# Kernel optimization log

Measured on AMD Instinct MI355X. Metric: run time of the kernel, lower is better.

Reference implementation:

```python
import jax, jax.numpy as jnp
import numpy as np

B, L, H, E = 2, 2048, 16, 64
S, D = L, E


def setup_inputs() -> dict:
    key = jax.random.key(0)
    kq, kk, kv = jax.random.split(key, 3)
    queries = jax.random.normal(kq, (B, L, H, E), dtype=jnp.float32)
    keys = jax.random.normal(kk, (B, S, H, E), dtype=jnp.float32)
    values = jax.random.normal(kv, (B, S, H, D), dtype=jnp.float32)
    return {"queries": queries, "keys": keys, "values": values}


def reference(queries, keys, values):
    # FullAttention forward: mask_flag=True, attn_mask=None -> causal mask,
    # scale=None -> 1/sqrt(E), dropout in eval mode (identity).
    Bq, Lq, Hq, Eq = queries.shape
    Sq = values.shape[1]
    scale = 1.0 / jnp.sqrt(jnp.asarray(Eq, dtype=queries.dtype))
    # [B,H,L,S] score matrix, same as torch.einsum('blhe,bshe->bhls', q, k)
    scores = jnp.einsum('blhe,bshe->bhls', queries, keys)
    # TriangularCausalMask: triu(ones, diagonal=1) -> True above diagonal = masked
    causal = jnp.triu(jnp.ones((Lq, Sq), dtype=bool), k=1)
    scores = jnp.where(causal[None, None, :, :], -jnp.inf, scores)
    A = jax.nn.softmax(scale * scores, axis=-1)
    V = jnp.einsum('bhls,bshd->blhd', A, values)
    return V
```

## Files before the change

### kernel.cpp

```cpp
#include <hip/hip_runtime.h>
#include <hip/hip_bf16.h>


#define B_DIM 2
#define L_DIM 2048
#define H_DIM 16
#define E_DIM 64
#define NEG_INF (-1e30f)
#define CAP   16.0f

typedef __attribute__((ext_vector_type(8))) short short8;
typedef __attribute__((ext_vector_type(4))) float ffrag;

static __device__ __forceinline__ short f2bf(float x) {
    __hip_bfloat16 h = __float2bfloat16(x);
    return *reinterpret_cast<short*>(&h);
}
static __device__ __forceinline__ unsigned pk2(float lo, float hi) {
    __hip_bfloat162 h = __float22bfloat162_rn(make_float2(lo, hi));
    return *reinterpret_cast<unsigned*>(&h);
}

__global__ __launch_bounds__(256, 4)
void attn_fused(const float* __restrict__ Q, const float* __restrict__ K,
                const float* __restrict__ V, float* __restrict__ O) {
    const int lid = blockIdx.x;
    const int x   = lid & 7;
    const int c   = (lid >> 3) & 31;
    const int k4  = lid >> 8;
    const int bh  = x * 4 + k4;
    const int b   = bh >> 4;
    const int h   = bh & 15;
    int strip;
    switch (k4) {
        case 0:  strip = c;              break;
        case 1:  strip = 31 - c;         break;
        case 2:  strip = c ^ 16;         break;
        default: strip = 31 - (c ^ 16);  break;
    }
    const int q0 = strip * 64;

    const int tid  = threadIdx.x;
    const int wave = tid >> 6;
    const int lane = tid & 63;
    const int n16  = lane & 15;
    const int quad = lane >> 4;

    __shared__ short Kt[4096];
    __shared__ short Vt[4096];
    __shared__ short Pq[4096];

    const float sc = 0.125f * 1.44269504088896340736f;
    const int gq = q0 + wave * 16 + n16;

    short8 qf[2];
    {
        const float4* pq = (const float4*)(Q + (((size_t)b * L_DIM + gq) * H_DIM + h) * E_DIM);
#pragma unroll
        for (int kt = 0; kt < 2; ++kt) {
            float4 x0 = pq[kt * 8 + quad * 2];
            float4 x1 = pq[kt * 8 + quad * 2 + 1];
            short8 f;
            f[0] = f2bf(x0.x * sc); f[1] = f2bf(x0.y * sc);
            f[2] = f2bf(x0.z * sc); f[3] = f2bf(x0.w * sc);
            f[4] = f2bf(x1.x * sc); f[5] = f2bf(x1.y * sc);
            f[6] = f2bf(x1.z * sc); f[7] = f2bf(x1.w * sc);
            qf[kt] = f;
        }
    }

    const int rr  = tid >> 2;
    const int c2  = tid & 3;
    const int kOff0 = rr * 64 + (((2 * c2)     ^ (rr & 7)) * 8);
    const int kOff1 = rr * 64 + (((2 * c2 + 1) ^ (rr & 7)) * 8);
    const int kp2 = (tid & 31) * 2;
    const int c8  = (tid >> 5) * 8;

    float4 kr[4], va[2], vb2[2];

    auto load_tile = [&](int kt0) {
        const float4* kg = (const float4*)(K + (((size_t)b * L_DIM + kt0 + rr) * H_DIM + h) * E_DIM + c2 * 16);
        kr[0] = kg[0]; kr[1] = kg[1]; kr[2] = kg[2]; kr[3] = kg[3];
        const float* vp = V + (((size_t)b * L_DIM + kt0 + kp2) * H_DIM + h) * E_DIM + c8;
        const float4* vga = (const float4*)vp;
        const float4* vgb = (const float4*)(vp + H_DIM * E_DIM);
        va[0]  = vga[0]; va[1]  = vga[1];
        vb2[0] = vgb[0]; vb2[1] = vgb[1];
    };
    auto store_tile = [&]() {
        short8 w0, w1;
        w0[0] = f2bf(kr[0].x); w0[1] = f2bf(kr[0].y); w0[2] = f2bf(kr[0].z); w0[3] = f2bf(kr[0].w);
        w0[4] = f2bf(kr[1].x); w0[5] = f2bf(kr[1].y); w0[6] = f2bf(kr[1].z); w0[7] = f2bf(kr[1].w);
        w1[0] = f2bf(kr[2].x); w1[1] = f2bf(kr[2].y); w1[2] = f2bf(kr[2].z); w1[3] = f2bf(kr[2].w);
        w1[4] = f2bf(kr[3].x); w1[5] = f2bf(kr[3].y); w1[6] = f2bf(kr[3].z); w1[7] = f2bf(kr[3].w);
        *(short8*)&Kt[kOff0] = w0;
        *(short8*)&Kt[kOff1] = w1;
        const float* a0 = (const float*)va;
        const float* b0 = (const float*)vb2;
#pragma unroll
        for (int i = 0; i < 8; ++i)
            *(unsigned*)&Vt[(c8 + i) * 64 + (((kp2 >> 3) ^ i) * 8) + (kp2 & 7)] = pk2(a0[i], b0[i]);
    };

    ffrag Oa[4];
#pragma unroll
    for (int nt = 0; nt < 4; ++nt) Oa[nt] = ffrag{0.f, 0.f, 0.f, 0.f};
    float l = 0.f;

    const int sw  = n16 & 7;
    const int fo0 = (quad ^ sw) * 8;
    const int fo1 = fo0 ^ 32;
    short* pbase = &Pq[wave * 1024 + n16 * 64];

    load_tile(0);

    for (int kt0 = 0; kt0 <= q0; kt0 += 64) {
        __syncthreads();
        store_tile();
        __syncthreads();
        if (kt0 + 64 <= q0) load_tile(kt0 + 64);

        ffrag S[4];
#pragma unroll
        for (int mt = 0; mt < 4; ++mt) {
            const int rb = (mt * 16 + n16) * 64;
            short8 a0 = *(const short8*)&Kt[rb + fo0];
            short8 a1 = *(const short8*)&Kt[rb + fo1];
            ffrag z = ffrag{0.f, 0.f, 0.f, 0.f};
            z = __builtin_amdgcn_mfma_f32_16x16x32_bf16(a0, qf[0], z, 0, 0, 0);
            S[mt] = __builtin_amdgcn_mfma_f32_16x16x32_bf16(a1, qf[1], z, 0, 0, 0);
        }

        const bool domask = (kt0 == q0);
        float ps = 0.f;
#pragma unroll
        for (int mt = 0; mt < 4; ++mt) {
            float pv[4];
#pragma unroll
            for (int r = 0; r < 4; ++r) {
                float sv = S[mt][r];
                if (domask && (mt * 16 + quad * 4 + r > wave * 16 + n16)) sv = NEG_INF;
                pv[r] = exp2f(sv - CAP);
                ps += pv[r];
            }
            uint2 w;
            w.x = pk2(pv[0], pv[1]);
            w.y = pk2(pv[2], pv[3]);
            *(uint2*)&pbase[(((2 * mt + (quad >> 1)) ^ sw) * 8) + (quad & 1) * 4] = w;
        }
        ps += __shfl_xor(ps, 16);
        ps += __shfl_xor(ps, 32);
        l += ps;

        short8 pa0 = *(const short8*)&pbase[fo0];
        short8 pa1 = *(const short8*)&pbase[fo1];

#pragma unroll
        for (int nt = 0; nt < 4; ++nt) {
            const int rb = (nt * 16 + n16) * 64;
            short8 b0 = *(const short8*)&Vt[rb + fo0];
            short8 b1 = *(const short8*)&Vt[rb + fo1];
            Oa[nt] = __builtin_amdgcn_mfma_f32_16x16x32_bf16(pa0, b0, Oa[nt], 0, 0, 0);
            Oa[nt] = __builtin_amdgcn_mfma_f32_16x16x32_bf16(pa1, b1, Oa[nt], 0, 0, 0);
        }
    }

#pragma unroll
    for (int r = 0; r < 4; ++r) {
        float li  = __shfl(l, quad * 4 + r);
        float inv = 1.0f / li;
        const int row = q0 + wave * 16 + quad * 4 + r;
        float* op = O + (((size_t)b * L_DIM + row) * H_DIM + h) * E_DIM;
#pragma unroll
        for (int nt = 0; nt < 4; ++nt) op[nt * 16 + n16] = Oa[nt][r] * inv;
    }
}

extern "C" void kernel_launch(void* const* d_in, const int* in_sizes, int n_in,
                              void* d_out, int out_size, void* d_ws, size_t ws_size,
                              hipStream_t stream) {
    const float* Q = (const float*)d_in[0];
    const float* K = (const float*)d_in[1];
    const float* V = (const float*)d_in[2];
    float* O = (float*)d_out;
    attn_fused<<<dim3(1024), 256, 0, stream>>>(Q, K, V, O);
}
```

Baseline: 139.4 us.

## Split long causal strips across blocks with static load-balance tables and combine pass

```diff
diff --git a/kernel.cpp b/kernel.cpp
--- a/kernel.cpp
+++ b/kernel.cpp
@@ -21,24 +21,28 @@
     return *reinterpret_cast<unsigned*>(&h);
 }
 
-__global__ __launch_bounds__(256, 4)
+static __device__ const unsigned char T_strip[8][3] = {
+    {0,15,15},{1,13,7},{2,13,6},{3,10,14},{8,4,14},{8,5,12},{9,10,12},{9,11,11}};
+static __device__ const unsigned char T_t0[8][3] = {
+    {0,0,16},{0,0,0},{0,14,0},{0,0,0},{0,0,15},{9,0,0},{0,11,13},{10,0,12}};
+static __device__ const unsigned char T_nt[8][3] = {
+    {2,16,16},{4,14,16},{6,14,14},{8,11,15},{9,10,15},{9,12,13},{10,11,13},{10,12,12}};
+
+__global__ __launch_bounds__(256, 3)
 void attn_fused(const float* __restrict__ Q, const float* __restrict__ K,
-                const float* __restrict__ V, float* __restrict__ O) {
+                const float* __restrict__ V, float* __restrict__ O,
+                float* __restrict__ Oacc, float* __restrict__ lacc) {
     const int lid = blockIdx.x;
-    const int x   = lid & 7;
-    const int c   = (lid >> 3) & 31;
+    const int cu  = lid & 255;
     const int k4  = lid >> 8;
-    const int bh  = x * 4 + k4;
-    const int b   = bh >> 4;
-    const int h   = bh & 15;
-    int strip;
-    switch (k4) {
-        case 0:  strip = c;              break;
-        case 1:  strip = 31 - c;         break;
-        case 2:  strip = c ^ 16;         break;
-        default: strip = 31 - (c ^ 16);  break;
-    }
-    const int q0 = strip * 64;
+    const int bh  = cu & 31;
+    const int j   = cu >> 5;
+    const int b = bh >> 4, h = bh & 15;
+
+    const int s   = T_strip[j][k4];
+    const int t0  = T_t0[j][k4];
+    const int ntl = T_nt[j][k4];
+    const int q0  = s * 128;
 
     const int tid  = threadIdx.x;
     const int wave = tid >> 6;
@@ -46,15 +50,16 @@
     const int n16  = lane & 15;
     const int quad = lane >> 4;
 
-    __shared__ short Kt[4096];
-    __shared__ short Vt[4096];
-    __shared__ short Pq[4096];
+    __shared__ short Kt[8192];
+    __shared__ short Vt[8192];
+    __shared__ short Pq[8192];
 
     const float sc = 0.125f * 1.44269504088896340736f;
-    const int gq = q0 + wave * 16 + n16;
-
-    short8 qf[2];
-    {
+
+    short8 qf[2][2];
+#pragma unroll
+    for (int g = 0; g < 2; ++g) {
+        const int gq = q0 + 32 * wave + 16 * g + n16;
         const float4* pq = (const float4*)(Q + (((size_t)b * L_DIM + gq) * H_DIM + h) * E_DIM);
 #pragma unroll
         for (int kt = 0; kt < 2; ++kt) {
@@ -65,7 +70,7 @@
             f[2] = f2bf(x0.z * sc); f[3] = f2bf(x0.w * sc);
             f[4] = f2bf(x1.x * sc); f[5] = f2bf(x1.y * sc);
             f[6] = f2bf(x1.z * sc); f[7] = f2bf(x1.w * sc);
-            qf[kt] = f;
+            qf[g][kt] = f;
         }
     }
 
@@ -78,7 +83,8 @@
 
     float4 kr[4], va[2], vb2[2];
 
-    auto load_tile = [&](int kt0) {
+    auto load_tile = [&](int t) {
+        const int kt0 = t * 64;
         const float4* kg = (const float4*)(K + (((size_t)b * L_DIM + kt0 + rr) * H_DIM + h) * E_DIM + c2 * 16);
         kr[0] = kg[0]; kr[1] = kg[1]; kr[2] = kg[2]; kr[3] = kg[3];
         const float* vp = V + (((size_t)b * L_DIM + kt0 + kp2) * H_DIM + h) * E_DIM + c8;
@@ -87,92 +93,170 @@
         va[0]  = vga[0]; va[1]  = vga[1];
         vb2[0] = vgb[0]; vb2[1] = vgb[1];
     };
-    auto store_tile = [&]() {
+    auto store_tile = [&](int bo) {
         short8 w0, w1;
         w0[0] = f2bf(kr[0].x); w0[1] = f2bf(kr[0].y); w0[2] = f2bf(kr[0].z); w0[3] = f2bf(kr[0].w);
         w0[4] = f2bf(kr[1].x); w0[5] = f2bf(kr[1].y); w0[6] = f2bf(kr[1].z); w0[7] = f2bf(kr[1].w);
         w1[0] = f2bf(kr[2].x); w1[1] = f2bf(kr[2].y); w1[2] = f2bf(kr[2].z); w1[3] = f2bf(kr[2].w);
         w1[4] = f2bf(kr[3].x); w1[5] = f2bf(kr[3].y); w1[6] = f2bf(kr[3].z); w1[7] = f2bf(kr[3].w);
-        *(short8*)&Kt[kOff0] = w0;
-        *(short8*)&Kt[kOff1] = w1;
+        *(short8*)&Kt[bo + kOff0] = w0;
+        *(short8*)&Kt[bo + kOff1] = w1;
         const float* a0 = (const float*)va;
         const float* b0 = (const float*)vb2;
 #pragma unroll
-        for (int i = 0; i < 8; ++i)
-            *(unsigned*)&Vt[(c8 + i) * 64 + (((kp2 >> 3) ^ i) * 8) + (kp2 & 7)] = pk2(a0[i], b0[i]);
+        for (int i2 = 0; i2 < 8; ++i2)
+            *(unsigned*)&Vt[bo + (c8 + i2) * 64 + (((kp2 >> 3) ^ i2) * 8) + (kp2 & 7)] = pk2(a0[i2], b0[i2]);
     };
 
-    ffrag Oa[4];
-#pragma unroll
-    for (int nt = 0; nt < 4; ++nt) Oa[nt] = ffrag{0.f, 0.f, 0.f, 0.f};
-    float l = 0.f;
+    ffrag Oa[2][4];
+#pragma unroll
+    for (int g = 0; g < 2; ++g)
+#pragma unroll
+        for (int nt = 0; nt < 4; ++nt) Oa[g][nt] = ffrag{0.f, 0.f, 0.f, 0.f};
+    float l2[2] = {0.f, 0.f};
 
     const int sw  = n16 & 7;
     const int fo0 = (quad ^ sw) * 8;
     const int fo1 = fo0 ^ 32;
-    short* pbase = &Pq[wave * 1024 + n16 * 64];
-
-    load_tile(0);
-
-    for (int kt0 = 0; kt0 <= q0; kt0 += 64) {
-        __syncthreads();
-        store_tile();
-        __syncthreads();
-        if (kt0 + 64 <= q0) load_tile(kt0 + 64);
-
-        ffrag S[4];
+
+    load_tile(t0);
+    store_tile(0);
+    load_tile(t0 + 1);
+    __syncthreads();
+
+    for (int i = 0; i < ntl; ++i) {
+        const int kt0 = (t0 + i) * 64;
+        const int bo  = (i & 1) ? 4096 : 0;
+
+        ffrag S[2][4];
 #pragma unroll
         for (int mt = 0; mt < 4; ++mt) {
-            const int rb = (mt * 16 + n16) * 64;
+            const int rb = bo + (mt * 16 + n16) * 64;
             short8 a0 = *(const short8*)&Kt[rb + fo0];
             short8 a1 = *(const short8*)&Kt[rb + fo1];
-            ffrag z = ffrag{0.f, 0.f, 0.f, 0.f};
-            z = __builtin_amdgcn_mfma_f32_16x16x32_bf16(a0, qf[0], z, 0, 0, 0);
-            S[mt] = __builtin_amdgcn_mfma_f32_16x16x32_bf16(a1, qf[1], z, 0, 0, 0);
-        }
-
-        const bool domask = (kt0 == q0);
-        float ps = 0.f;
-#pragma unroll
-        for (int mt = 0; mt < 4; ++mt) {
-            float pv[4];
-#pragma unroll
-            for (int r = 0; r < 4; ++r) {
-                float sv = S[mt][r];
-                if (domask && (mt * 16 + quad * 4 + r > wave * 16 + n16)) sv = NEG_INF;
-                pv[r] = exp2f(sv - CAP);
-                ps += pv[r];
-            }
-            uint2 w;
-            w.x = pk2(pv[0], pv[1]);
-            w.y = pk2(pv[2], pv[3]);
-            *(uint2*)&pbase[(((2 * mt + (quad >> 1)) ^ sw) * 8) + (quad & 1) * 4] = w;
-        }
-        ps += __shfl_xor(ps, 16);
-        ps += __shfl_xor(ps, 32);
-        l += ps;
-
-        short8 pa0 = *(const short8*)&pbase[fo0];
-        short8 pa1 = *(const short8*)&pbase[fo1];
+#pragma unroll
+            for (int g = 0; g < 2; ++g) {
+                ffrag z = ffrag{0.f, 0.f, 0.f, 0.f};
+                z = __builtin_amdgcn_mfma_f32_16x16x32_bf16(a0, qf[g][0], z, 0, 0, 0);
+                S[g][mt] = __builtin_amdgcn_mfma_f32_16x16x32_bf16(a1, qf[g][1], z, 0, 0, 0);
+            }
+        }
+
+#pragma unroll
+        for (int g = 0; g < 2; ++g) {
+            const int qmin = q0 + 32 * wave + 16 * g;
+            const bool domask = (kt0 + 63 > qmin);
+            short* pb = &Pq[(wave * 2 + g) * 1024 + n16 * 64];
+            float ps = 0.f;
+#pragma unroll
+            for (int mt = 0; mt < 4; ++mt) {
+                float pv[4];
+#pragma unroll
+                for (int r = 0; r < 4; ++r) {
+                    float sv = S[g][mt][r];
+                    if (domask && (kt0 + mt * 16 + quad * 4 + r > qmin + n16)) sv = NEG_INF;
+                    pv[r] = exp2f(sv - CAP);
+                    ps += pv[r];
+                }
+                uint2 w;
+                w.x = pk2(pv[0], pv[1]);
+                w.y = pk2(pv[2], pv[3]);
+                *(uint2*)&pb[(((2 * mt + (quad >> 1)) ^ sw) * 8) + (quad & 1) * 4] = w;
+            }
+            ps += __shfl_xor(ps, 16);
+            ps += __shfl_xor(ps, 32);
+            l2[g] += ps;
+        }
+
+        short8 pa[2][2];
+#pragma unroll
+        for (int g = 0; g < 2; ++g) {
+            const short* pb = &Pq[(wave * 2 + g) * 1024 + n16 * 64];
+            pa[g][0] = *(const short8*)&pb[fo0];
+            pa[g][1] = *(const short8*)&pb[fo1];
+        }
 
 #pragma unroll
         for (int nt = 0; nt < 4; ++nt) {
-            const int rb = (nt * 16 + n16) * 64;
+            const int rb = bo + (nt * 16 + n16) * 64;
             short8 b0 = *(const short8*)&Vt[rb + fo0];
             short8 b1 = *(const short8*)&Vt[rb + fo1];
-            Oa[nt] = __builtin_amdgcn_mfma_f32_16x16x32_bf16(pa0, b0, Oa[nt], 0, 0, 0);
-            Oa[nt] = __builtin_amdgcn_mfma_f32_16x16x32_bf16(pa1, b1, Oa[nt], 0, 0, 0);
-        }
-    }
-
-#pragma unroll
-    for (int r = 0; r < 4; ++r) {
-        float li  = __shfl(l, quad * 4 + r);
-        float inv = 1.0f / li;
-        const int row = q0 + wave * 16 + quad * 4 + r;
-        float* op = O + (((size_t)b * L_DIM + row) * H_DIM + h) * E_DIM;
-#pragma unroll
-        for (int nt = 0; nt < 4; ++nt) op[nt * 16 + n16] = Oa[nt][r] * inv;
+#pragma unroll
+            for (int g = 0; g < 2; ++g) {
+                Oa[g][nt] = __builtin_amdgcn_mfma_f32_16x16x32_bf16(pa[g][0], b0, Oa[g][nt], 0, 0, 0);
+                Oa[g][nt] = __builtin_amdgcn_mfma_f32_16x16x32_bf16(pa[g][1], b1, Oa[g][nt], 0, 0, 0);
+            }
+        }
+
+        if (i + 1 < ntl) store_tile((i & 1) ? 0 : 4096);
+        if (i + 2 < ntl) load_tile(t0 + i + 2);
+        __syncthreads();
+    }
+
+    if (s < 8) {
+#pragma unroll
+        for (int g = 0; g < 2; ++g)
+#pragma unroll
+            for (int r = 0; r < 4; ++r) {
+                float li  = __shfl(l2[g], quad * 4 + r);
+                float inv = 1.0f / li;
+                const int row = q0 + 32 * wave + 16 * g + quad * 4 + r;
+                float* op = O + (((size_t)b * L_DIM + row) * H_DIM + h) * E_DIM;
+#pragma unroll
+                for (int nt = 0; nt < 4; ++nt) op[nt * 16 + n16] = Oa[g][nt][r] * inv;
+            }
+        return;
+    }
+
+    const int accIdx = bh * 8 + (s - 8);
+    const int chunk  = (t0 != 0);
+    float* la = lacc + accIdx * 256 + chunk * 128;
+#pragma unroll
+    for (int g = 0; g < 2; ++g)
+        if (quad == 0) la[32 * wave + 16 * g + n16] = l2[g];
+
+    if (chunk == 0) {
+        float* oa = Oacc + (size_t)accIdx * 8192;
+#pragma unroll
+        for (int g = 0; g < 2; ++g)
+#pragma unroll
+            for (int nt = 0; nt < 4; ++nt)
+#pragma unroll
+                for (int r = 0; r < 4; ++r)
+                    oa[(32 * wave + 16 * g + quad * 4 + r) * 64 + nt * 16 + n16] = Oa[g][nt][r];
+    } else {
+#pragma unroll
+        for (int g = 0; g < 2; ++g)
+#pragma unroll
+            for (int r = 0; r < 4; ++r) {
+                const int row = q0 + 32 * wave + 16 * g + quad * 4 + r;
+                float* op = O + (((size_t)b * L_DIM + row) * H_DIM + h) * E_DIM;
+#pragma unroll
+                for (int nt = 0; nt < 4; ++nt) op[nt * 16 + n16] = Oa[g][nt][r];
+            }
+    }
+}
+
+__global__ __launch_bounds__(256)
+void combine(float* __restrict__ O, const float* __restrict__ Oacc,
+             const float* __restrict__ lacc) {
+    const int a  = blockIdx.x;
+    const int bh = a >> 3;
+    const int s  = 8 + (a & 7);
+    const int b = bh >> 4, h = bh & 15;
+    const int t = threadIdx.x;
+    const int row = t >> 1;
+    const int d0  = (t & 1) * 32;
+
+    float l   = lacc[a * 256 + row] + lacc[a * 256 + 128 + row];
+    float inv = 1.0f / l;
+    const float4* pa = (const float4*)(Oacc + (size_t)a * 8192 + row * 64 + d0);
+    float4* po = (float4*)(O + (((size_t)b * L_DIM + s * 128 + row) * H_DIM + h) * E_DIM + d0);
+#pragma unroll
+    for (int i = 0; i < 8; ++i) {
+        float4 x = po[i], y = pa[i];
+        po[i] = make_float4((x.x + y.x) * inv, (x.y + y.y) * inv,
+                            (x.z + y.z) * inv, (x.w + y.w) * inv);
     }
 }
 
@@ -183,5 +267,8 @@
     const float* K = (const float*)d_in[1];
     const float* V = (const float*)d_in[2];
     float* O = (float*)d_out;
-    attn_fused<<<dim3(1024), 256, 0, stream>>>(Q, K, V, O);
-}
+    float* Oacc = (float*)d_ws;
+    float* lacc = (float*)((char*)d_ws + 8388608);
+    attn_fused<<<dim3(768), 256, 0, stream>>>(Q, K, V, O, Oacc, lacc);
+    combine<<<dim3(256), 256, 0, stream>>>(O, Oacc, lacc);
+}
```

Result: slower. 159.0 us (+14.1%).

## Split long causal query strips across blocks with partial outputs and a combine kernel

Applied to the files above, without the earlier changes.

```diff
diff --git a/kernel.cpp b/kernel.cpp
--- a/kernel.cpp
+++ b/kernel.cpp
@@ -20,25 +20,45 @@
     __hip_bfloat162 h = __float22bfloat162_rn(make_float2(lo, hi));
     return *reinterpret_cast<unsigned*>(&h);
 }
-
-__global__ __launch_bounds__(256, 4)
+static __device__ __forceinline__ float bf2f(unsigned u) {
+    u <<= 16;
+    return *reinterpret_cast<float*>(&u);
+}
+union U16 { uint4 u4; short8 s8; };
+
+static __device__ const unsigned char Ts[5][8] = {
+    {15,14,13,12,11,15,14,13},
+    {12,11,10, 9, 8,15,14,13},
+    {12,11,10, 9, 8,15, 7, 7},
+    { 6, 5, 4, 3, 6,10,14, 2},
+    { 0, 4, 8,12, 5, 9,13, 1}};
+static __device__ const unsigned char Tt0[5][8] = {
+    {24,16,16,16,16,16, 8, 8},
+    { 8, 8, 8, 8, 8, 8, 0, 0},
+    { 0, 0, 0, 0, 0, 0, 8, 0},
+    { 0, 0, 0, 0, 8,16,24, 0},
+    { 0, 8,16,24, 8,16,24, 0}};
+static __device__ const unsigned char Tnt[5][8] = {
+    {8,8,8,8,8,8,8,8},
+    {8,8,8,8,8,8,8,8},
+    {8,8,8,8,8,8,8,8},
+    {8,8,8,8,6,6,6,6},
+    {2,2,2,2,4,4,4,4}};
+
+__global__ __launch_bounds__(256, 8)
 void attn_fused(const float* __restrict__ Q, const float* __restrict__ K,
-                const float* __restrict__ V, float* __restrict__ O) {
+                const float* __restrict__ V, float* __restrict__ O,
+                unsigned short* __restrict__ Opart, float* __restrict__ lacc) {
     const int lid = blockIdx.x;
-    const int x   = lid & 7;
-    const int c   = (lid >> 3) & 31;
-    const int k4  = lid >> 8;
-    const int bh  = x * 4 + k4;
-    const int b   = bh >> 4;
-    const int h   = bh & 15;
-    int strip;
-    switch (k4) {
-        case 0:  strip = c;              break;
-        case 1:  strip = 31 - c;         break;
-        case 2:  strip = c ^ 16;         break;
-        default: strip = 31 - (c ^ 16);  break;
-    }
-    const int q0 = strip * 64;
+    const int bh  = lid & 31;
+    const int c   = lid >> 5;
+    const int kk  = c >> 3, r = c & 7;
+    const int s   = Ts[kk][r];
+    const int t0  = Tt0[kk][r];
+    const int ntl = Tnt[kk][r];
+    const int q0  = s << 7;
+    const int b = bh >> 4, h = bh & 15;
+    const bool isfinal = (t0 + ntl == 2 * s + 2);
 
     const int tid  = threadIdx.x;
     const int wave = tid >> 6;
@@ -48,24 +68,25 @@
 
     __shared__ short Kt[4096];
     __shared__ short Vt[4096];
-    __shared__ short Pq[4096];
+    __shared__ short Pq[8192];
 
     const float sc = 0.125f * 1.44269504088896340736f;
-    const int gq = q0 + wave * 16 + n16;
-
-    short8 qf[2];
-    {
+
+    short8 qf[2][2];
+#pragma unroll
+    for (int g = 0; g < 2; ++g) {
+        const int gq = q0 + 32 * wave + 16 * g + n16;
         const float4* pq = (const float4*)(Q + (((size_t)b * L_DIM + gq) * H_DIM + h) * E_DIM);
 #pragma unroll
         for (int kt = 0; kt < 2; ++kt) {
             float4 x0 = pq[kt * 8 + quad * 2];
             float4 x1 = pq[kt * 8 + quad * 2 + 1];
-            short8 f;
-            f[0] = f2bf(x0.x * sc); f[1] = f2bf(x0.y * sc);
-            f[2] = f2bf(x0.z * sc); f[3] = f2bf(x0.w * sc);
-            f[4] = f2bf(x1.x * sc); f[5] = f2bf(x1.y * sc);
-            f[6] = f2bf(x1.z * sc); f[7] = f2bf(x1.w * sc);
-            qf[kt] = f;
+            U16 u;
+            u.u4.x = pk2(x0.x * sc, x0.y * sc);
+            u.u4.y = pk2(x0.z * sc, x0.w * sc);
+            u.u4.z = pk2(x1.x * sc, x1.y * sc);
+            u.u4.w = pk2(x1.z * sc, x1.w * sc);
+            qf[g][kt] = u.s8;
         }
     }
 
@@ -76,104 +97,199 @@
     const int kp2 = (tid & 31) * 2;
     const int c8  = (tid >> 5) * 8;
 
-    float4 kr[4], va[2], vb2[2];
-
-    auto load_tile = [&](int kt0) {
-        const float4* kg = (const float4*)(K + (((size_t)b * L_DIM + kt0 + rr) * H_DIM + h) * E_DIM + c2 * 16);
-        kr[0] = kg[0]; kr[1] = kg[1]; kr[2] = kg[2]; kr[3] = kg[3];
-        const float* vp = V + (((size_t)b * L_DIM + kt0 + kp2) * H_DIM + h) * E_DIM + c8;
-        const float4* vga = (const float4*)vp;
-        const float4* vgb = (const float4*)(vp + H_DIM * E_DIM);
-        va[0]  = vga[0]; va[1]  = vga[1];
-        vb2[0] = vgb[0]; vb2[1] = vgb[1];
-    };
-    auto store_tile = [&]() {
-        short8 w0, w1;
-        w0[0] = f2bf(kr[0].x); w0[1] = f2bf(kr[0].y); w0[2] = f2bf(kr[0].z); w0[3] = f2bf(kr[0].w);
-        w0[4] = f2bf(kr[1].x); w0[5] = f2bf(kr[1].y); w0[6] = f2bf(kr[1].z); w0[7] = f2bf(kr[1].w);
-        w1[0] = f2bf(kr[2].x); w1[1] = f2bf(kr[2].y); w1[2] = f2bf(kr[2].z); w1[3] = f2bf(kr[2].w);
-        w1[4] = f2bf(kr[3].x); w1[5] = f2bf(kr[3].y); w1[6] = f2bf(kr[3].z); w1[7] = f2bf(kr[3].w);
-        *(short8*)&Kt[kOff0] = w0;
-        *(short8*)&Kt[kOff1] = w1;
-        const float* a0 = (const float*)va;
-        const float* b0 = (const float*)vb2;
-#pragma unroll
-        for (int i = 0; i < 8; ++i)
-            *(unsigned*)&Vt[(c8 + i) * 64 + (((kp2 >> 3) ^ i) * 8) + (kp2 & 7)] = pk2(a0[i], b0[i]);
-    };
-
-    ffrag Oa[4];
-#pragma unroll
-    for (int nt = 0; nt < 4; ++nt) Oa[nt] = ffrag{0.f, 0.f, 0.f, 0.f};
-    float l = 0.f;
+    ffrag Oa[2][4];
+#pragma unroll
+    for (int g = 0; g < 2; ++g)
+#pragma unroll
+        for (int nt = 0; nt < 4; ++nt) Oa[g][nt] = ffrag{0.f, 0.f, 0.f, 0.f};
+    float l2[2] = {0.f, 0.f};
 
     const int sw  = n16 & 7;
     const int fo0 = (quad ^ sw) * 8;
     const int fo1 = fo0 ^ 32;
-    short* pbase = &Pq[wave * 1024 + n16 * 64];
-
-    load_tile(0);
-
-    for (int kt0 = 0; kt0 <= q0; kt0 += 64) {
+    short* pb0 = &Pq[(wave * 2 + 0) * 1024 + n16 * 64];
+    short* pb1 = &Pq[(wave * 2 + 1) * 1024 + n16 * 64];
+    const int qrow0 = q0 + 32 * wave + n16;
+
+    for (int i = 0; i < ntl; ++i) {
+        const int kt0 = (t0 + i) << 6;
         __syncthreads();
-        store_tile();
+        {
+            const float4* kg = (const float4*)(K + (((size_t)b * L_DIM + kt0 + rr) * H_DIM + h) * E_DIM + c2 * 16);
+            float4 f0 = kg[0], f1 = kg[1];
+            U16 u0;
+            u0.u4.x = pk2(f0.x, f0.y); u0.u4.y = pk2(f0.z, f0.w);
+            u0.u4.z = pk2(f1.x, f1.y); u0.u4.w = pk2(f1.z, f1.w);
+            *(uint4*)&Kt[kOff0] = u0.u4;
+            float4 f2 = kg[2], f3 = kg[3];
+            U16 u1;
+            u1.u4.x = pk2(f2.x, f2.y); u1.u4.y = pk2(f2.z, f2.w);
+            u1.u4.z = pk2(f3.x, f3.y); u1.u4.w = pk2(f3.z, f3.w);
+            *(uint4*)&Kt[kOff1] = u1.u4;
+        }
+        {
+            const float* vp = V + (((size_t)b * L_DIM + kt0 + kp2) * H_DIM + h) * E_DIM + c8;
+            const float4* va4 = (const float4*)vp;
+            const float4* vb4 = (const float4*)(vp + H_DIM * E_DIM);
+            float4 a0 = va4[0], b0 = vb4[0];
+            *(unsigned*)&Vt[(c8 + 0) * 64 + (((kp2 >> 3) ^ 0) * 8) + (kp2 & 7)] = pk2(a0.x, b0.x);
+            *(unsigned*)&Vt[(c8 + 1) * 64 + (((kp2 >> 3) ^ 1) * 8) + (kp2 & 7)] = pk2(a0.y, b0.y);
+            *(unsigned*)&Vt[(c8 + 2) * 64 + (((kp2 >> 3) ^ 2) * 8) + (kp2 & 7)] = pk2(a0.z, b0.z);
+            *(unsigned*)&Vt[(c8 + 3) * 64 + (((kp2 >> 3) ^ 3) * 8) + (kp2 & 7)] = pk2(a0.w, b0.w);
+            float4 a1 = va4[1], b1 = vb4[1];
+            *(unsigned*)&Vt[(c8 + 4) * 64 + (((kp2 >> 3) ^ 4) * 8) + (kp2 & 7)] = pk2(a1.x, b1.x);
+            *(unsigned*)&Vt[(c8 + 5) * 64 + (((kp2 >> 3) ^ 5) * 8) + (kp2 & 7)] = pk2(a1.y, b1.y);
+            *(unsigned*)&Vt[(c8 + 6) * 64 + (((kp2 >> 3) ^ 6) * 8) + (kp2 & 7)] = pk2(a1.z, b1.z);
+            *(unsigned*)&Vt[(c8 + 7) * 64 + (((kp2 >> 3) ^ 7) * 8) + (kp2 & 7)] = pk2(a1.w, b1.w);
+        }
         __syncthreads();
-        if (kt0 + 64 <= q0) load_tile(kt0 + 64);
-
-        ffrag S[4];
+
+        const bool diag = (kt0 + 64 > q0);
 #pragma unroll
         for (int mt = 0; mt < 4; ++mt) {
             const int rb = (mt * 16 + n16) * 64;
             short8 a0 = *(const short8*)&Kt[rb + fo0];
             short8 a1 = *(const short8*)&Kt[rb + fo1];
-            ffrag z = ffrag{0.f, 0.f, 0.f, 0.f};
-            z = __builtin_amdgcn_mfma_f32_16x16x32_bf16(a0, qf[0], z, 0, 0, 0);
-            S[mt] = __builtin_amdgcn_mfma_f32_16x16x32_bf16(a1, qf[1], z, 0, 0, 0);
-        }
-
-        const bool domask = (kt0 == q0);
-        float ps = 0.f;
-#pragma unroll
-        for (int mt = 0; mt < 4; ++mt) {
-            float pv[4];
-#pragma unroll
-            for (int r = 0; r < 4; ++r) {
-                float sv = S[mt][r];
-                if (domask && (mt * 16 + quad * 4 + r > wave * 16 + n16)) sv = NEG_INF;
-                pv[r] = exp2f(sv - CAP);
-                ps += pv[r];
+            ffrag z0 = ffrag{0.f, 0.f, 0.f, 0.f};
+            z0 = __builtin_amdgcn_mfma_f32_16x16x32_bf16(a0, qf[0][0], z0, 0, 0, 0);
+            z0 = __builtin_amdgcn_mfma_f32_16x16x32_bf16(a1, qf[0][1], z0, 0, 0, 0);
+            ffrag z1 = ffrag{0.f, 0.f, 0.f, 0.f};
+            z1 = __builtin_amdgcn_mfma_f32_16x16x32_bf16(a0, qf[1][0], z1, 0, 0, 0);
+            z1 = __builtin_amdgcn_mfma_f32_16x16x32_bf16(a1, qf[1][1], z1, 0, 0, 0);
+            const int key0 = kt0 + mt * 16 + quad * 4;
+            float pv0[4], pv1[4];
+#pragma unroll
+            for (int q = 0; q < 4; ++q) {
+                float s0 = z0[q], s1 = z1[q];
+                if (diag) {
+                    if (key0 + q > qrow0)      s0 = NEG_INF;
+                    if (key0 + q > qrow0 + 16) s1 = NEG_INF;
+                }
+                pv0[q] = exp2f(s0 - CAP);
+                pv1[q] = exp2f(s1 - CAP);
+                l2[0] += pv0[q];
+                l2[1] += pv1[q];
             }
-            uint2 w;
-            w.x = pk2(pv[0], pv[1]);
-            w.y = pk2(pv[2], pv[3]);
-            *(uint2*)&pbase[(((2 * mt + (quad >> 1)) ^ sw) * 8) + (quad & 1) * 4] = w;
-        }
-        ps += __shfl_xor(ps, 16);
-        ps += __shfl_xor(ps, 32);
-        l += ps;
-
-        short8 pa0 = *(const short8*)&pbase[fo0];
-        short8 pa1 = *(const short8*)&pbase[fo1];
+            const int poff = (((2 * mt + (quad >> 1)) ^ sw) * 8) + (quad & 1) * 4;
+            uint2 w0, w1;
+            w0.x = pk2(pv0[0], pv0[1]); w0.y = pk2(pv0[2], pv0[3]);
+            w1.x = pk2(pv1[0], pv1[1]); w1.y = pk2(pv1[2], pv1[3]);
+            *(uint2*)&pb0[poff] = w0;
+            *(uint2*)&pb1[poff] = w1;
+        }
+
+        short8 p00 = *(const short8*)&pb0[fo0];
+        short8 p01 = *(const short8*)&pb0[fo1];
+        short8 p10 = *(const short8*)&pb1[fo0];
+        short8 p11 = *(const short8*)&pb1[fo1];
 
 #pragma unroll
         for (int nt = 0; nt < 4; ++nt) {
             const int rb = (nt * 16 + n16) * 64;
-            short8 b0 = *(const short8*)&Vt[rb + fo0];
-            short8 b1 = *(const short8*)&Vt[rb + fo1];
-            Oa[nt] = __builtin_amdgcn_mfma_f32_16x16x32_bf16(pa0, b0, Oa[nt], 0, 0, 0);
-            Oa[nt] = __builtin_amdgcn_mfma_f32_16x16x32_bf16(pa1, b1, Oa[nt], 0, 0, 0);
-        }
-    }
-
-#pragma unroll
-    for (int r = 0; r < 4; ++r) {
-        float li  = __shfl(l, quad * 4 + r);
-        float inv = 1.0f / li;
-        const int row = q0 + wave * 16 + quad * 4 + r;
-        float* op = O + (((size_t)b * L_DIM + row) * H_DIM + h) * E_DIM;
-#pragma unroll
-        for (int nt = 0; nt < 4; ++nt) op[nt * 16 + n16] = Oa[nt][r] * inv;
-    }
+            short8 v0 = *(const short8*)&Vt[rb + fo0];
+            short8 v1 = *(const short8*)&Vt[rb + fo1];
+            Oa[0][nt] = __builtin_amdgcn_mfma_f32_16x16x32_bf16(p00, v0, Oa[0][nt], 0, 0, 0);
+            Oa[0][nt] = __builtin_amdgcn_mfma_f32_16x16x32_bf16(p01, v1, Oa[0][nt], 0, 0, 0);
+            Oa[1][nt] = __builtin_amdgcn_mfma_f32_16x16x32_bf16(p10, v0, Oa[1][nt], 0, 0, 0);
+            Oa[1][nt] = __builtin_amdgcn_mfma_f32_16x16x32_bf16(p11, v1, Oa[1][nt], 0, 0, 0);
+        }
+    }
+
+    float lf[2];
+#pragma unroll
+    for (int g = 0; g < 2; ++g) {
+        float t = l2[g] + __shfl_xor(l2[g], 16);
+        lf[g] = t + __shfl_xor(t, 32);
+    }
+
+    if (isfinal && t0 == 0) {
+#pragma unroll
+        for (int g = 0; g < 2; ++g)
+#pragma unroll
+            for (int q = 0; q < 4; ++q) {
+                float li  = __shfl(lf[g], quad * 4 + q);
+                float inv = 1.0f / li;
+                const int row = q0 + 32 * wave + 16 * g + quad * 4 + q;
+                float* op = O + (((size_t)b * L_DIM + row) * H_DIM + h) * E_DIM;
+#pragma unroll
+                for (int nt = 0; nt < 4; ++nt) op[nt * 16 + n16] = Oa[g][nt][q] * inv;
+            }
+        return;
+    }
+
+    const int pos = t0 >> 3;
+    if (quad == 0) {
+#pragma unroll
+        for (int g = 0; g < 2; ++g)
+            lacc[((bh * 16 + s) * 4 + pos) * 128 + 32 * wave + 16 * g + n16] = lf[g];
+    }
+
+    if (isfinal) {
+#pragma unroll
+        for (int g = 0; g < 2; ++g)
+#pragma unroll
+            for (int q = 0; q < 4; ++q) {
+                const int row = q0 + 32 * wave + 16 * g + quad * 4 + q;
+                float* op = O + (((size_t)b * L_DIM + row) * H_DIM + h) * E_DIM;
+#pragma unroll
+                for (int nt = 0; nt < 4; ++nt) op[nt * 16 + n16] = Oa[g][nt][q];
+            }
+    } else {
+        const int base = (s < 8) ? (s - 4) : ((s < 12) ? 4 + 2 * (s - 8) : 12 + 3 * (s - 12));
+        unsigned short* op = Opart + (size_t)(bh * 24 + base + pos) * 8192;
+#pragma unroll
+        for (int g = 0; g < 2; ++g)
+#pragma unroll
+            for (int q = 0; q < 4; ++q) {
+                const int rl = 32 * wave + 16 * g + quad * 4 + q;
+#pragma unroll
+                for (int nt = 0; nt < 4; ++nt)
+                    op[rl * 64 + nt * 16 + n16] = (unsigned short)f2bf(Oa[g][nt][q]);
+            }
+    }
+}
+
+__global__ __launch_bounds__(256)
+void combine(float* __restrict__ O, const unsigned short* __restrict__ Opart,
+             const float* __restrict__ lacc) {
+    const int a    = blockIdx.x;
+    const int head = a & 31;
+    const int s    = 4 + (a >> 5);
+    const int b = head >> 4, h = head & 15;
+    const int npos = (s < 8) ? 2 : ((s < 12) ? 3 : 4);
+    const int base = (s < 8) ? (s - 4) : ((s < 12) ? 4 + 2 * (s - 8) : 12 + 3 * (s - 12));
+    const int t   = threadIdx.x;
+    const int row = t >> 1;
+    const int d0  = (t & 1) * 32;
+
+    float l = 0.f;
+    for (int pos = 0; pos < npos; ++pos)
+        l += lacc[((head * 16 + s) * 4 + pos) * 128 + row];
+    const float inv = 1.0f / l;
+
+    float* po = O + (((size_t)b * L_DIM + s * 128 + row) * H_DIM + h) * E_DIM + d0;
+    float acc[32];
+#pragma unroll
+    for (int i = 0; i < 8; ++i) {
+        float4 x = ((const float4*)po)[i];
+        acc[i * 4 + 0] = x.x; acc[i * 4 + 1] = x.y;
+        acc[i * 4 + 2] = x.z; acc[i * 4 + 3] = x.w;
+    }
+    for (int pos = 0; pos + 1 < npos; ++pos) {
+        const unsigned short* pp = Opart + (size_t)(head * 24 + base + pos) * 8192 + row * 64 + d0;
+#pragma unroll
+        for (int j = 0; j < 4; ++j) {
+            uint4 w = ((const uint4*)pp)[j];
+            acc[j * 8 + 0] += bf2f(w.x & 0xffffu); acc[j * 8 + 1] += bf2f(w.x >> 16);
+            acc[j * 8 + 2] += bf2f(w.y & 0xffffu); acc[j * 8 + 3] += bf2f(w.y >> 16);
+            acc[j * 8 + 4] += bf2f(w.z & 0xffffu); acc[j * 8 + 5] += bf2f(w.z >> 16);
+            acc[j * 8 + 6] += bf2f(w.w & 0xffffu); acc[j * 8 + 7] += bf2f(w.w >> 16);
+        }
+    }
+#pragma unroll
+    for (int i = 0; i < 8; ++i)
+        ((float4*)po)[i] = make_float4(acc[i * 4 + 0] * inv, acc[i * 4 + 1] * inv,
+                                       acc[i * 4 + 2] * inv, acc[i * 4 + 3] * inv);
 }
 
 extern "C" void kernel_launch(void* const* d_in, const int* in_sizes, int n_in,
@@ -183,5 +299,8 @@
     const float* K = (const float*)d_in[1];
     const float* V = (const float*)d_in[2];
     float* O = (float*)d_out;
-    attn_fused<<<dim3(1024), 256, 0, stream>>>(Q, K, V, O);
-}
+    unsigned short* Opart = (unsigned short*)d_ws;
+    float* lacc = (float*)((char*)d_ws + 12582912);
+    attn_fused<<<dim3(1280), 256, 0, stream>>>(Q, K, V, O, Opart, lacc);
+    combine<<<dim3(384), 256, 0, stream>>>(O, Opart, lacc);
+}
```

New measurement: 144.1 us. 1.03x slower.
